# Optimization experiments

Measured on AMD Instinct MI355X. Metric: run time of the kernel, lower is better.

## Reference

```python
import jax, jax.numpy as jnp
import numpy as np
import math

B, S, E, H = 2, 2048, 1024, 16


def setup_inputs() -> dict:
    key = jax.random.key(0)
    ks = jax.random.split(key, 9)
    std = 0.02
    return {
        "x": jax.random.normal(ks[0], (B, S, E), dtype=jnp.float32),
        "Wq": jax.random.normal(ks[1], (E, E), dtype=jnp.float32) * std,
        "bq": jnp.zeros((E,), dtype=jnp.float32),
        "Wk": jax.random.normal(ks[2], (E, E), dtype=jnp.float32) * std,
        "bk": jnp.zeros((E,), dtype=jnp.float32),
        "Wv": jax.random.normal(ks[3], (E, E), dtype=jnp.float32) * std,
        "bv": jnp.zeros((E,), dtype=jnp.float32),
        "Wfc": jax.random.normal(ks[4], (E, E), dtype=jnp.float32) * std,
        "bfc": jnp.zeros((E,), dtype=jnp.float32),
        "n_head": H,
    }


def reference(x, Wq, bq, Wk, bk, Wv, bv, Wfc, bfc, n_head):
    Bn, Sn, En = x.shape
    Hd = En // n_head  # head_dim
    # torch Linear: y = x @ W.T + b
    def proj(W, b):
        return (x @ W.T + b).reshape(Bn, Sn, n_head, Hd).transpose(0, 2, 1, 3)  # [B,H,S,D]
    q = proj(Wq, bq)
    k = proj(Wk, bk)
    v = proj(Wv, bv)
    scores = jnp.einsum('bhqd,bhkd->bhqk', q, k) / math.sqrt(Hd)  # [B,H,S,S]
    # ALiBi: slopes_h = 2^{-(h+1)}; alibi[h,i,j] = -slope_h * (i - j)
    slopes = 2.0 ** (-jnp.arange(1, n_head + 1, dtype=jnp.float32))  # [H]
    pos = jnp.arange(Sn, dtype=jnp.float32)
    rel = pos[:, None] - pos[None, :]  # [S,S], memory_pos - context_pos
    alibi = -slopes[:, None, None] * rel  # [H,S,S]
    scores = scores + alibi[None]
    weights = jax.nn.softmax(scores, axis=-1)  # [B,H,S,S]
    out = jnp.einsum('bhqk,bhkd->bqhd', weights, v).reshape(Bn, Sn, En)
    out = out @ Wfc.T + bfc
    return (out, weights)
```

## Files before the change

kernel.cpp:

```cpp
#include <hip/hip_runtime.h>
#include <hip/hip_bf16.h>
#include <cstdint>
#include <cstddef>

#define BB 2
#define SS 2048
#define EE 1024
#define HH 16
#define MM (BB*SS)

typedef __bf16 bf16;
typedef __bf16 bf16x8 __attribute__((ext_vector_type(8)));
typedef float f32x4 __attribute__((ext_vector_type(4)));

#define GLD16(gsrc, ldst) \
  __builtin_amdgcn_global_load_lds((const __attribute__((address_space(1))) void*)(gsrc), \
                                   (__attribute__((address_space(3))) void*)(ldst), 16, 0, 0)

__global__ __launch_bounds__(256) void cvt_f32_bf16(const float* __restrict__ src,
                                                    bf16* __restrict__ dst, int n) {
    int i = (blockIdx.x * 256 + threadIdx.x) * 8;
    if (i >= n) return;
    float4 a = *(const float4*)(src + i);
    float4 b = *(const float4*)(src + i + 4);
    bf16 o[8] = {(bf16)a.x,(bf16)a.y,(bf16)a.z,(bf16)a.w,
                 (bf16)b.x,(bf16)b.y,(bf16)b.z,(bf16)b.w};
    *(uint4*)(dst + i) = *(uint4*)o;
}

__global__ __launch_bounds__(256) void cvt4(const float* __restrict__ a, const float* __restrict__ b,
                                            const float* __restrict__ c, const float* __restrict__ d,
                                            bf16* __restrict__ oa, bf16* __restrict__ ob,
                                            bf16* __restrict__ oc, bf16* __restrict__ od) {
    int sel = blockIdx.y;
    const float* s = sel == 0 ? a : sel == 1 ? b : sel == 2 ? c : d;
    bf16* o       = sel == 0 ? oa : sel == 1 ? ob : sel == 2 ? oc : od;
    int i = (blockIdx.x * 256 + threadIdx.x) * 8;
    float4 x = *(const float4*)(s + i);
    float4 y = *(const float4*)(s + i + 4);
    bf16 t[8] = {(bf16)x.x,(bf16)x.y,(bf16)x.z,(bf16)x.w,
                 (bf16)y.x,(bf16)y.y,(bf16)y.z,(bf16)y.w};
    *(uint4*)(o + i) = *(uint4*)t;
}

template<int MODE>
__global__ __launch_bounds__(256) void gemm128(const bf16* __restrict__ A,
                                               const bf16* __restrict__ W0,
                                               const bf16* __restrict__ W1,
                                               const bf16* __restrict__ W2,
                                               const float* __restrict__ b0,
                                               const float* __restrict__ b1,
                                               const float* __restrict__ b2,
                                               void* __restrict__ o0,
                                               void* __restrict__ o1,
                                               void* __restrict__ o2) {
    __shared__ bf16 Al[128*64];
    __shared__ bf16 Bl[128*64];
    const int t = threadIdx.x;
    const int wsel = blockIdx.x >> 3;
    const int n0 = (blockIdx.x & 7) * 128;
    const int m0 = blockIdx.y * 128;
    const bf16* W  = wsel == 0 ? W0 : wsel == 1 ? W1 : W2;
    const float* bias = wsel == 0 ? b0 : wsel == 1 ? b1 : b2;
    void* outp = wsel == 0 ? o0 : wsel == 1 ? o1 : o2;

    const int w = t >> 6, lane = t & 63, lg = lane >> 4, li = lane & 15;
    const int wr = w >> 1, wc = w & 1;
    f32x4 acc[4][4] = {};

    for (int k0 = 0; k0 < 1024; k0 += 64) {
        __syncthreads();
        #pragma unroll
        for (int i = 0; i < 4; ++i) {
            int f = i * 256 + t;
            int row = f >> 3, c = (f & 7) * 8;
            GLD16(A + (size_t)(m0 + row) * 1024 + k0 + c, Al + f * 8);
            GLD16(W + (size_t)(n0 + row) * 1024 + k0 + c, Bl + f * 8);
        }
        __syncthreads();
        #pragma unroll
        for (int ks = 0; ks < 2; ++ks) {
            bf16x8 af[4], bf_[4];
            #pragma unroll
            for (int m = 0; m < 4; ++m)
                af[m] = *(const bf16x8*)&Al[(wr*64 + m*16 + li)*64 + ks*32 + lg*8];
            #pragma unroll
            for (int n = 0; n < 4; ++n)
                bf_[n] = *(const bf16x8*)&Bl[(wc*64 + n*16 + li)*64 + ks*32 + lg*8];
            #pragma unroll
            for (int m = 0; m < 4; ++m)
                #pragma unroll
                for (int n = 0; n < 4; ++n)
                    acc[m][n] = __builtin_amdgcn_mfma_f32_16x16x32_bf16(af[m], bf_[n], acc[m][n], 0,0,0);
        }
    }
    #pragma unroll
    for (int m = 0; m < 4; ++m)
      #pragma unroll
      for (int n = 0; n < 4; ++n)
        #pragma unroll
        for (int r = 0; r < 4; ++r) {
            int row = m0 + wr*64 + m*16 + lg*4 + r;
            int col = n0 + wc*64 + n*16 + li;
            float v = acc[m][n][r] + bias[col];
            if (MODE == 0) {
                int b = row >> 11, s = row & (SS-1);
                int h = col >> 6, d = col & 63;
                ((bf16*)outp)[(((size_t)(b*HH + h)*SS + s) << 6) + d] = (bf16)v;
            } else {
                ((float*)outp)[(size_t)row*1024 + col] = v;
            }
        }
}

__global__ __launch_bounds__(256) void transpose_v(const bf16* __restrict__ V,
                                                   bf16* __restrict__ Vt) {
    __shared__ bf16 L[64][72];
    const int bh = blockIdx.y, s0 = blockIdx.x * 64, t = threadIdx.x;
    for (int id = t; id < 512; id += 256) {
        int row = id >> 3, c = id & 7;
        *(uint4*)&L[row][c*8] = *(const uint4*)&V[((size_t)bh*SS + s0 + row)*64 + c*8];
    }
    __syncthreads();
    for (int id = t; id < 512; id += 256) {
        int d = id >> 3, c = id & 7;
        bf16 tmp[8];
        #pragma unroll
        for (int jj = 0; jj < 8; ++jj) tmp[jj] = L[c*8 + jj][d];
        *(uint4*)&Vt[((size_t)bh*64 + d)*SS + s0 + c*8] = *(uint4*)tmp;
    }
}

__global__ __launch_bounds__(256) void attn_kernel(const bf16* __restrict__ Q,
                                                   const bf16* __restrict__ Kk,
                                                   const bf16* __restrict__ Vt,
                                                   float* __restrict__ wout,
                                                   bf16* __restrict__ aout) {
    __shared__ bf16 Ks[2][64*64];
    __shared__ bf16 Vs[2][64*64];
    __shared__ float Lred[2][64];

    const int lin = blockIdx.x + (int)(gridDim.x * blockIdx.y);
    const int nl  = (lin & 7) * 128 + (lin >> 3);
    const int qt = nl & 31, bh = nl >> 5;

    const int b = bh >> 4, h = bh & 15;
    const int q0 = qt * 64;
    const int t = threadIdx.x, w = t >> 6, lane = t & 63, lg = lane >> 4, li = lane & 15;
    const int jh = w & 1, qh = w >> 1;
    const float slope = exp2f(-(float)(h + 1));
    const size_t kvbase = (size_t)bh * SS * 64;
    const size_t vtbase = (size_t)bh * 64 * SS;
    const float L2E = 1.4426950408889634f;
    const float K1 = 0.125f * L2E;
    const float C  = slope * L2E;
    const float C64 = C * 64.f;

    bf16x8 aq[2][2];
    #pragma unroll
    for (int cbq = 0; cbq < 2; ++cbq) {
        const bf16* qptr = Q + kvbase + (size_t)(q0 + qh*32 + cbq*16 + li) * 64;
        aq[cbq][0] = *(const bf16x8*)(qptr + lg*8);
        aq[cbq][1] = *(const bf16x8*)(qptr + 32 + lg*8);
    }

    const int swz = (li & 7) << 4;

    float cj[2][4];
    #pragma unroll
    for (int jt = 0; jt < 2; ++jt)
        #pragma unroll
        for (int r = 0; r < 4; ++r)
            cj[jt][r] = C * (float)(jh*32 + jt*16 + lg*4 + r - (SS-1));
    float lp[2] = {0.f, 0.f};

    #pragma unroll
    for (int i = 0; i < 2; ++i) {
        int f = i*256 + t; int row = f >> 3, c16 = f & 7;
        GLD16(Kk + kvbase + (size_t)row*64 + (c16 ^ (row & 7))*8, &Ks[0][0] + f*8);
    }
    __syncthreads();
    for (int kt = 0; kt < 32; ++kt) {
        const int cur = kt & 1;
        if (kt + 1 < 32) {
            #pragma unroll
            for (int i = 0; i < 2; ++i) {
                int f = i*256 + t; int row = f >> 3, c16 = f & 7;
                GLD16(Kk + kvbase + (size_t)((kt+1)*64 + row)*64 + (c16 ^ (row & 7))*8,
                      &Ks[cur^1][0] + f*8);
            }
        }
        const char* Ksb = (const char*)&Ks[cur][0];
        bf16x8 ak[2][2];
        #pragma unroll
        for (int jt = 0; jt < 2; ++jt) {
            int row = jh*32 + jt*16 + li;
            ak[jt][0] = *(const bf16x8*)(Ksb + row*128 + ((     lg*16) ^ swz));
            ak[jt][1] = *(const bf16x8*)(Ksb + row*128 + ((64 + lg*16) ^ swz));
        }
        f32x4 sc[2][2] = {};
        __builtin_amdgcn_s_setprio(1);
        #pragma unroll
        for (int jt = 0; jt < 2; ++jt)
            #pragma unroll
            for (int cbq = 0; cbq < 2; ++cbq) {
                sc[jt][cbq] = __builtin_amdgcn_mfma_f32_16x16x32_bf16(ak[jt][0], aq[cbq][0], sc[jt][cbq], 0,0,0);
                sc[jt][cbq] = __builtin_amdgcn_mfma_f32_16x16x32_bf16(ak[jt][1], aq[cbq][1], sc[jt][cbq], 0,0,0);
            }
        __builtin_amdgcn_s_setprio(0);
        #pragma unroll
        for (int jt = 0; jt < 2; ++jt) {
            #pragma unroll
            for (int cbq = 0; cbq < 2; ++cbq)
                #pragma unroll
                for (int r = 0; r < 4; ++r)
                    lp[cbq] += __builtin_amdgcn_exp2f(fmaf(sc[jt][cbq][r], K1, cj[jt][r]));
            #pragma unroll
            for (int r = 0; r < 4; ++r) cj[jt][r] += C64;
        }
        __syncthreads();
    }
    #pragma unroll
    for (int cbq = 0; cbq < 2; ++cbq) {
        lp[cbq] += __shfl_xor(lp[cbq], 16);
        lp[cbq] += __shfl_xor(lp[cbq], 32);
    }
    if (lg == 0) {
        Lred[jh][qh*32 + li]      = lp[0];
        Lred[jh][qh*32 + 16 + li] = lp[1];
    }
    #pragma unroll
    for (int i = 0; i < 2; ++i) {
        int f = i*256 + t; int row = f >> 3, c16 = f & 7;
        GLD16(Kk + kvbase + (size_t)row*64 + (c16 ^ (row & 7))*8, &Ks[0][0] + f*8);
        GLD16(Vt + vtbase + (size_t)row*SS + (c16 ^ (row & 7))*8, &Vs[0][0] + f*8);
    }
    __syncthreads();
    float lgl[2];
    #pragma unroll
    for (int cbq = 0; cbq < 2; ++cbq) {
        int qi = qh*32 + cbq*16 + li;
        lgl[cbq] = __builtin_amdgcn_logf(Lred[0][qi] + Lred[1][qi]);
    }
    float ecr[2][2][4];
    #pragma unroll
    for (int jt = 0; jt < 2; ++jt)
        #pragma unroll
        for (int cbq = 0; cbq < 2; ++cbq)
            #pragma unroll
            for (int r = 0; r < 4; ++r)
                ecr[jt][cbq][r] = C * (float)(jh*32 + jt*16 + lg*4 + r - (SS-1)) - lgl[cbq];

    f32x4 acc[2][4] = {};
    float* wrow0 = wout + ((size_t)bh*SS + q0 + qh*32 +      li) * SS;
    float* wrow1 = wout + ((size_t)bh*SS + q0 + qh*32 + 16 + li) * SS;

    for (int kt = 0; kt < 32; ++kt) {
        const int cur = kt & 1;
        const int j0 = kt * 64;
        if (kt + 1 < 32) {
            #pragma unroll
            for (int i = 0; i < 2; ++i) {
                int f = i*256 + t; int row = f >> 3, c16 = f & 7;
                GLD16(Kk + kvbase + (size_t)(j0 + 64 + row)*64 + (c16 ^ (row & 7))*8,
                      &Ks[cur^1][0] + f*8);
                GLD16(Vt + vtbase + (size_t)row*SS + j0 + 64 + (c16 ^ (row & 7))*8,
                      &Vs[cur^1][0] + f*8);
            }
        }
        const char* Ksb = (const char*)&Ks[cur][0];
        const char* Vsb = (const char*)&Vs[cur][0];
        bf16x8 ak[2][2];
        #pragma unroll
        for (int jt = 0; jt < 2; ++jt) {
            int row = jh*32 + jt*16 + li;
            ak[jt][0] = *(const bf16x8*)(Ksb + row*128 + ((     lg*16) ^ swz));
            ak[jt][1] = *(const bf16x8*)(Ksb + row*128 + ((64 + lg*16) ^ swz));
        }
        f32x4 sc[2][2] = {};
        __builtin_amdgcn_s_setprio(1);
        #pragma unroll
        for (int jt = 0; jt < 2; ++jt)
            #pragma unroll
            for (int cbq = 0; cbq < 2; ++cbq) {
                sc[jt][cbq] = __builtin_amdgcn_mfma_f32_16x16x32_bf16(ak[jt][0], aq[cbq][0], sc[jt][cbq], 0,0,0);
                sc[jt][cbq] = __builtin_amdgcn_mfma_f32_16x16x32_bf16(ak[jt][1], aq[cbq][1], sc[jt][cbq], 0,0,0);
            }
        __builtin_amdgcn_s_setprio(0);
        float4 wv[2][2];
        #pragma unroll
        for (int jt = 0; jt < 2; ++jt)
            #pragma unroll
            for (int cbq = 0; cbq < 2; ++cbq) {
                float4 v;
                v.x = __builtin_amdgcn_exp2f(fmaf(sc[jt][cbq][0], K1, ecr[jt][cbq][0]));
                v.y = __builtin_amdgcn_exp2f(fmaf(sc[jt][cbq][1], K1, ecr[jt][cbq][1]));
                v.z = __builtin_amdgcn_exp2f(fmaf(sc[jt][cbq][2], K1, ecr[jt][cbq][2]));
                v.w = __builtin_amdgcn_exp2f(fmaf(sc[jt][cbq][3], K1, ecr[jt][cbq][3]));
                wv[jt][cbq] = v;
                float* wr = (cbq == 0 ? wrow0 : wrow1);
                *(float4*)&wr[j0 + jh*32 + jt*16 + lg*4] = v;
                ecr[jt][cbq][0] += C64; ecr[jt][cbq][1] += C64;
                ecr[jt][cbq][2] += C64; ecr[jt][cbq][3] += C64;
            }
        bf16x8 pa[2];
        #pragma unroll
        for (int cbq = 0; cbq < 2; ++cbq) {
            bf16x8 p;
            p[0] = (bf16)wv[0][cbq].x; p[1] = (bf16)wv[0][cbq].y;
            p[2] = (bf16)wv[0][cbq].z; p[3] = (bf16)wv[0][cbq].w;
            p[4] = (bf16)wv[1][cbq].x; p[5] = (bf16)wv[1][cbq].y;
            p[6] = (bf16)wv[1][cbq].z; p[7] = (bf16)wv[1][cbq].w;
            pa[cbq] = p;
        }
        bf16x8 vb[4];
        #pragma unroll
        for (int d0 = 0; d0 < 4; ++d0) {
            int row = d0*16 + li;
            uint2 u0 = *(const uint2*)(Vsb + row*128 + ((jh*64      + lg*8) ^ swz));
            uint2 u1 = *(const uint2*)(Vsb + row*128 + ((jh*64 + 32 + lg*8) ^ swz));
            uint4 uu = {u0.x, u0.y, u1.x, u1.y};
            vb[d0] = __builtin_bit_cast(bf16x8, uu);
        }
        __builtin_amdgcn_s_setprio(1);
        #pragma unroll
        for (int cbq = 0; cbq < 2; ++cbq)
            #pragma unroll
            for (int d0 = 0; d0 < 4; ++d0)
                acc[cbq][d0] = __builtin_amdgcn_mfma_f32_16x16x32_bf16(pa[cbq], vb[d0], acc[cbq][d0], 0,0,0);
        __builtin_amdgcn_s_setprio(0);
        __syncthreads();
    }

    bf16* Obuf = &Ks[0][0];
    #pragma unroll
    for (int cbq = 0; cbq < 2; ++cbq)
        #pragma unroll
        for (int d0 = 0; d0 < 4; ++d0)
            #pragma unroll
            for (int r = 0; r < 4; ++r)
                Obuf[jh*4096 + (qh*32 + cbq*16 + lg*4 + r)*64 + d0*16 + li] =
                    (bf16)acc[cbq][d0][r];
    __syncthreads();
    {
        int q = t >> 2, dc = (t & 3) << 4;
        const bf16* o0 = Obuf +        q*64 + dc;
        const bf16* o1 = Obuf + 4096 + q*64 + dc;
        bf16x8 a0 = *(const bf16x8*)(o0),     a1 = *(const bf16x8*)(o0 + 8);
        bf16x8 b0 = *(const bf16x8*)(o1),     b1 = *(const bf16x8*)(o1 + 8);
        bf16 ov[16];
        #pragma unroll
        for (int e = 0; e < 8; ++e) {
            ov[e]     = (bf16)((float)a0[e] + (float)b0[e]);
            ov[8 + e] = (bf16)((float)a1[e] + (float)b1[e]);
        }
        bf16* dst = aout + ((size_t)(b*SS + q0 + q))*EE + h*64 + dc;
        *(uint4*)(dst)     = *(uint4*)(ov);
        *(uint4*)(dst + 8) = *(uint4*)(ov + 8);
    }
}

extern "C" void kernel_launch(void* const* d_in, const int* in_sizes, int n_in,
                              void* d_out, int out_size, void* d_ws, size_t ws_size,
                              hipStream_t stream) {
    const float* x   = (const float*)d_in[0];
    const float* Wq  = (const float*)d_in[1];
    const float* bq  = (const float*)d_in[2];
    const float* Wk  = (const float*)d_in[3];
    const float* bk  = (const float*)d_in[4];
    const float* Wv  = (const float*)d_in[5];
    const float* bv  = (const float*)d_in[6];
    const float* Wfc = (const float*)d_in[7];
    const float* bfc = (const float*)d_in[8];

    char* ws = (char*)d_ws;
    const size_t MB = 1024u*1024u;
    bf16* xb  = (bf16*)(ws + 0);
    bf16* wqb = (bf16*)(ws + 8*MB);
    bf16* wkb = (bf16*)(ws + 10*MB);
    bf16* wvb = (bf16*)(ws + 12*MB);
    bf16* wfb = (bf16*)(ws + 14*MB);
    bf16* Qb  = (bf16*)(ws + 16*MB);
    bf16* Kb  = (bf16*)(ws + 24*MB);
    bf16* Vb  = (bf16*)(ws + 32*MB);
    bf16* Vtb = (bf16*)(ws + 40*MB);
    bf16* Ab  = (bf16*)(ws + 48*MB);

    float* outp = (float*)d_out;
    float* wout = outp + (size_t)BB*SS*EE;

    cvt_f32_bf16<<<dim3(4194304/8/256), 256, 0, stream>>>(x, xb, 4194304);
    cvt4<<<dim3(512, 4), 256, 0, stream>>>(Wq, Wk, Wv, Wfc, wqb, wkb, wvb, wfb);

    gemm128<0><<<dim3(24, 32), 256, 0, stream>>>(xb, wqb, wkb, wvb, bq, bk, bv, Qb, Kb, Vb);

    transpose_v<<<dim3(SS/64, BB*HH), 256, 0, stream>>>(Vb, Vtb);

    attn_kernel<<<dim3(32, 32), 256, 0, stream>>>(Qb, Kb, Vtb, wout, Ab);

    gemm128<1><<<dim3(8, 32), 256, 0, stream>>>(Ab, wfb, wfb, wfb, bfc, bfc, bfc, d_out, d_out, d_out);
}
```

Measured before the change: 307.3 us.

## Deepen K prefetch ring, use explicit vmcnt barriers and nontemporal weight stores

Replaces the separate double-buffered K/V LDS arrays with one four-slot ring. The first (normalizer) pass now prefetches K two tiles ahead. The `__syncthreads` calls become explicit `s_waitcnt vmcnt(N)` waits plus raw barriers, so outstanding global traffic, including the output stores, need not drain every iteration. The large fp32 attention-weights writes become nontemporal stores to reduce cache pollution. In exchange, correctness now depends on hand-counted vmcnt values matching the issue order of loads and stores.

```diff
diff --git a/kernel.cpp b/kernel.cpp
--- a/kernel.cpp
+++ b/kernel.cpp
@@ -16,6 +16,11 @@
 #define GLD16(gsrc, ldst) \
   __builtin_amdgcn_global_load_lds((const __attribute__((address_space(1))) void*)(gsrc), \
                                    (__attribute__((address_space(3))) void*)(ldst), 16, 0, 0)
+
+#define VMWAIT(N) do { asm volatile("s_waitcnt vmcnt(" #N ")" ::: "memory"); \
+                       __builtin_amdgcn_sched_barrier(0); } while (0)
+#define XBAR() do { __builtin_amdgcn_s_barrier(); \
+                    __builtin_amdgcn_sched_barrier(0); } while (0)
 
 __global__ __launch_bounds__(256) void cvt_f32_bf16(const float* __restrict__ src,
                                                     bf16* __restrict__ dst, int n) {
@@ -136,8 +141,7 @@
                                                    const bf16* __restrict__ Vt,
                                                    float* __restrict__ wout,
                                                    bf16* __restrict__ aout) {
-    __shared__ bf16 Ks[2][64*64];
-    __shared__ bf16 Vs[2][64*64];
+    __shared__ bf16 ring[4][64*64];
     __shared__ float Lred[2][64];
 
     const int lin = blockIdx.x + (int)(gridDim.x * blockIdx.y);
@@ -166,6 +170,21 @@
 
     const int swz = (li & 7) << 4;
 
+    #define STAGE_K(J0, DST) do {                                              \
+        _Pragma("unroll")                                                      \
+        for (int i_ = 0; i_ < 2; ++i_) {                                       \
+            int f_ = i_*256 + t; int row_ = f_ >> 3, c_ = f_ & 7;              \
+            GLD16(Kk + kvbase + (size_t)((J0) + row_)*64 + (c_ ^ (row_ & 7))*8,\
+                  (DST) + f_*8);                                               \
+        } } while (0)
+    #define STAGE_V(J0, DST) do {                                              \
+        _Pragma("unroll")                                                      \
+        for (int i_ = 0; i_ < 2; ++i_) {                                       \
+            int f_ = i_*256 + t; int row_ = f_ >> 3, c_ = f_ & 7;              \
+            GLD16(Vt + vtbase + (size_t)row_*SS + (J0) + (c_ ^ (row_ & 7))*8,  \
+                  (DST) + f_*8);                                               \
+        } } while (0)
+
     float cj[2][4];
     #pragma unroll
     for (int jt = 0; jt < 2; ++jt)
@@ -174,23 +193,13 @@
             cj[jt][r] = C * (float)(jh*32 + jt*16 + lg*4 + r - (SS-1));
     float lp[2] = {0.f, 0.f};
 
-    #pragma unroll
-    for (int i = 0; i < 2; ++i) {
-        int f = i*256 + t; int row = f >> 3, c16 = f & 7;
-        GLD16(Kk + kvbase + (size_t)row*64 + (c16 ^ (row & 7))*8, &Ks[0][0] + f*8);
-    }
-    __syncthreads();
+    STAGE_K(0,  &ring[0][0]);
+    STAGE_K(64, &ring[1][0]);
+    VMWAIT(2);
+    XBAR();
     for (int kt = 0; kt < 32; ++kt) {
-        const int cur = kt & 1;
-        if (kt + 1 < 32) {
-            #pragma unroll
-            for (int i = 0; i < 2; ++i) {
-                int f = i*256 + t; int row = f >> 3, c16 = f & 7;
-                GLD16(Kk + kvbase + (size_t)((kt+1)*64 + row)*64 + (c16 ^ (row & 7))*8,
-                      &Ks[cur^1][0] + f*8);
-            }
-        }
-        const char* Ksb = (const char*)&Ks[cur][0];
+        if (kt + 2 < 32) STAGE_K((kt+2)*64, &ring[(kt+2) & 3][0]);
+        const char* Ksb = (const char*)&ring[kt & 3][0];
         bf16x8 ak[2][2];
         #pragma unroll
         for (int jt = 0; jt < 2; ++jt) {
@@ -218,7 +227,8 @@
             #pragma unroll
             for (int r = 0; r < 4; ++r) cj[jt][r] += C64;
         }
-        __syncthreads();
+        if (kt < 30) { VMWAIT(2); } else { VMWAIT(0); }
+        XBAR();
     }
     #pragma unroll
     for (int cbq = 0; cbq < 2; ++cbq) {
@@ -229,13 +239,11 @@
         Lred[jh][qh*32 + li]      = lp[0];
         Lred[jh][qh*32 + 16 + li] = lp[1];
     }
-    #pragma unroll
-    for (int i = 0; i < 2; ++i) {
-        int f = i*256 + t; int row = f >> 3, c16 = f & 7;
-        GLD16(Kk + kvbase + (size_t)row*64 + (c16 ^ (row & 7))*8, &Ks[0][0] + f*8);
-        GLD16(Vt + vtbase + (size_t)row*SS + (c16 ^ (row & 7))*8, &Vs[0][0] + f*8);
-    }
-    __syncthreads();
+    STAGE_K(0, &ring[0][0]);
+    STAGE_V(0, &ring[2][0]);
+    asm volatile("s_waitcnt vmcnt(0) lgkmcnt(0)" ::: "memory");
+    __builtin_amdgcn_sched_barrier(0);
+    XBAR();
     float lgl[2];
     #pragma unroll
     for (int cbq = 0; cbq < 2; ++cbq) {
@@ -259,17 +267,11 @@
         const int cur = kt & 1;
         const int j0 = kt * 64;
         if (kt + 1 < 32) {
-            #pragma unroll
-            for (int i = 0; i < 2; ++i) {
-                int f = i*256 + t; int row = f >> 3, c16 = f & 7;
-                GLD16(Kk + kvbase + (size_t)(j0 + 64 + row)*64 + (c16 ^ (row & 7))*8,
-                      &Ks[cur^1][0] + f*8);
-                GLD16(Vt + vtbase + (size_t)row*SS + j0 + 64 + (c16 ^ (row & 7))*8,
-                      &Vs[cur^1][0] + f*8);
-            }
-        }
-        const char* Ksb = (const char*)&Ks[cur][0];
-        const char* Vsb = (const char*)&Vs[cur][0];
+            STAGE_K(j0 + 64, &ring[cur ^ 1][0]);
+            STAGE_V(j0 + 64, &ring[2 + (cur ^ 1)][0]);
+        }
+        const char* Ksb = (const char*)&ring[cur][0];
+        const char* Vsb = (const char*)&ring[2 + cur][0];
         bf16x8 ak[2][2];
         #pragma unroll
         for (int jt = 0; jt < 2; ++jt) {
@@ -287,19 +289,19 @@
                 sc[jt][cbq] = __builtin_amdgcn_mfma_f32_16x16x32_bf16(ak[jt][1], aq[cbq][1], sc[jt][cbq], 0,0,0);
             }
         __builtin_amdgcn_s_setprio(0);
-        float4 wv[2][2];
+        f32x4 wv[2][2];
         #pragma unroll
         for (int jt = 0; jt < 2; ++jt)
             #pragma unroll
             for (int cbq = 0; cbq < 2; ++cbq) {
-                float4 v;
-                v.x = __builtin_amdgcn_exp2f(fmaf(sc[jt][cbq][0], K1, ecr[jt][cbq][0]));
-                v.y = __builtin_amdgcn_exp2f(fmaf(sc[jt][cbq][1], K1, ecr[jt][cbq][1]));
-                v.z = __builtin_amdgcn_exp2f(fmaf(sc[jt][cbq][2], K1, ecr[jt][cbq][2]));
-                v.w = __builtin_amdgcn_exp2f(fmaf(sc[jt][cbq][3], K1, ecr[jt][cbq][3]));
+                f32x4 v;
+                v[0] = __builtin_amdgcn_exp2f(fmaf(sc[jt][cbq][0], K1, ecr[jt][cbq][0]));
+                v[1] = __builtin_amdgcn_exp2f(fmaf(sc[jt][cbq][1], K1, ecr[jt][cbq][1]));
+                v[2] = __builtin_amdgcn_exp2f(fmaf(sc[jt][cbq][2], K1, ecr[jt][cbq][2]));
+                v[3] = __builtin_amdgcn_exp2f(fmaf(sc[jt][cbq][3], K1, ecr[jt][cbq][3]));
                 wv[jt][cbq] = v;
                 float* wr = (cbq == 0 ? wrow0 : wrow1);
-                *(float4*)&wr[j0 + jh*32 + jt*16 + lg*4] = v;
+                __builtin_nontemporal_store(v, (f32x4*)&wr[j0 + jh*32 + jt*16 + lg*4]);
                 ecr[jt][cbq][0] += C64; ecr[jt][cbq][1] += C64;
                 ecr[jt][cbq][2] += C64; ecr[jt][cbq][3] += C64;
             }
@@ -307,10 +309,10 @@
         #pragma unroll
         for (int cbq = 0; cbq < 2; ++cbq) {
             bf16x8 p;
-            p[0] = (bf16)wv[0][cbq].x; p[1] = (bf16)wv[0][cbq].y;
-            p[2] = (bf16)wv[0][cbq].z; p[3] = (bf16)wv[0][cbq].w;
-            p[4] = (bf16)wv[1][cbq].x; p[5] = (bf16)wv[1][cbq].y;
-            p[6] = (bf16)wv[1][cbq].z; p[7] = (bf16)wv[1][cbq].w;
+            p[0] = (bf16)wv[0][cbq][0]; p[1] = (bf16)wv[0][cbq][1];
+            p[2] = (bf16)wv[0][cbq][2]; p[3] = (bf16)wv[0][cbq][3];
+            p[4] = (bf16)wv[1][cbq][0]; p[5] = (bf16)wv[1][cbq][1];
+            p[6] = (bf16)wv[1][cbq][2]; p[7] = (bf16)wv[1][cbq][3];
             pa[cbq] = p;
         }
         bf16x8 vb[4];
@@ -329,10 +331,11 @@
             for (int d0 = 0; d0 < 4; ++d0)
                 acc[cbq][d0] = __builtin_amdgcn_mfma_f32_16x16x32_bf16(pa[cbq], vb[d0], acc[cbq][d0], 0,0,0);
         __builtin_amdgcn_s_setprio(0);
-        __syncthreads();
-    }
-
-    bf16* Obuf = &Ks[0][0];
+        VMWAIT(4);
+        XBAR();
+    }
+
+    bf16* Obuf = &ring[0][0];
     #pragma unroll
     for (int cbq = 0; cbq < 2; ++cbq)
         #pragma unroll
@@ -358,6 +361,8 @@
         *(uint4*)(dst)     = *(uint4*)(ov);
         *(uint4*)(dst + 8) = *(uint4*)(ov + 8);
     }
+    #undef STAGE_K
+    #undef STAGE_V
 }
 
 extern "C" void kernel_launch(void* const* d_in, const int* in_sizes, int n_in,
```

Result: faster. 299.8 us (-2.4%).
